# Kernel optimization log

Hardware: AMD Instinct MI355X
Metric: run time of the kernel (lower is better)

The kernel has to match this reference:

```python
import jax, jax.numpy as jnp
import numpy as np
import math

B, CH, BINS, W = 2, 8, 1024, 1024
FF = 2048
BANDS = 4
HD = BINS // BANDS
EPS = 1e-5


def _ln(x, g, b):
    m = jnp.mean(x, -1, keepdims=True)
    v = jnp.mean(jnp.square(x - m), -1, keepdims=True)
    return (x - m) * jax.lax.rsqrt(v + EPS) * g + b


def _conv1d(x, w, pad, groups=1):
    # x: [B, C, W], w: [O, I/groups, k]
    return jax.lax.conv_general_dilated(x, w, (1,), [(pad, pad)],
                                        dimension_numbers=('NCH', 'OIH', 'NCH'),
                                        feature_group_count=groups)


def _attn(h, mem, qw, qb, qcw, qcb, kw, kb, kcw, kcb, vw, vb, vcw, vcb, ow, ob, er):
    b, w, c = h.shape

    def proj(src, lw, lb, cw, cb):
        y = src @ lw.T + lb                                   # [b, w, c]
        y = _conv1d(y.transpose(0, 2, 1), cw, 1, groups=c) + cb[None, :, None]
        return y.transpose(0, 2, 1)                           # [b, w, c]

    q = proj(h, qw, qb, qcw, qcb).reshape(b, w, BANDS, HD).transpose(0, 2, 1, 3)   # [b, n, w, hd]
    k = proj(mem, kw, kb, kcw, kcb).reshape(b, w, BANDS, HD).transpose(0, 2, 1, 3)
    v = proj(mem, vw, vb, vcw, vcb).reshape(b, w, BANDS, HD).transpose(0, 2, 1, 3)
    # relative position bias via Music-Transformer pad/skew trick
    p = jnp.einsum('bnwh,hc->bnwc', q, er)                    # [b, n, w, W]
    p = jnp.pad(p, ((0, 0), (0, 0), (0, 0), (1, 0))).transpose(0, 1, 3, 2)[:, :, 1:, :]
    qk = (jnp.einsum('bnqh,bnkh->bnqk', q, k) + p) / math.sqrt(c)
    a = jax.nn.softmax(qk, axis=-1)
    o = jnp.einsum('bnqk,bnkh->bnqh', a, v).transpose(0, 2, 1, 3).reshape(b, w, c)
    return o @ ow.T + ob


def _forward(x, w_in, ln1_g, ln1_b, glu_w, ln2_g, ln2_b, c1L_w, c1R_w, ln3_g, ln3_b,
             c1M_dw, c1M_pw, ln4_g, ln4_b, qw, qb, qcw, qcb, kw, kb, kcw, kcb,
             vw, vb, vcw, vcb, ow, ob, er, ln5_g, ln5_b, c2_w, c3_w):
    # in_project: Linear(channels, 1, bias=False) on x.transpose(1,3), squeeze
    xf = jnp.einsum('bcfw,c->bwf', x, w_in)                   # [B, W, BINS]
    # GLU block
    h = _ln(xf, ln1_g, ln1_b)
    g = h @ glu_w.T
    ga, gb = jnp.split(g, 2, axis=-1)
    xf = xf + ga * jax.nn.sigmoid(gb)
    # conv feedforward block
    h = _ln(xf, ln2_g, ln2_b)
    hL = jax.nn.relu(h @ c1L_w.T)                             # [B, W, FF]
    hR = jax.nn.relu(_conv1d(h.transpose(0, 2, 1), c1R_w, 1)).transpose(0, 2, 1)  # [B, W, FF//4]
    hR = jnp.pad(hR, ((0, 0), (0, 0), (0, FF - FF // 4)))
    h = _ln(hL + hR, ln3_g, ln3_b)
    h = _conv1d(_conv1d(h.transpose(0, 2, 1), c1M_dw, 4, groups=FF), c1M_pw, 0).transpose(0, 2, 1)
    xf = xf + h
    # multiband attention
    h = _ln(xf, ln4_g, ln4_b)
    h = _attn(h, h, qw, qb, qcw, qcb, kw, kb, kcw, kcb, vw, vb, vcw, vcb, ow, ob, er)
    xf = xf + h
    # squared-relu FFN
    h = _ln(xf, ln5_g, ln5_b)
    h = jnp.square(jax.nn.relu(h @ c2_w.T)) @ c3_w.T
    xf = xf + h
    return xf.transpose(0, 2, 1)[:, None, :, :]               # [B, 1, BINS, W]


def setup_inputs() -> dict:
    key = jax.random.key(0)
    keys = iter(jax.random.split(key, 48))

    def n(shape, s=0.02):
        return jax.random.normal(next(keys), shape, dtype=jnp.float32) * s

    ones = lambda d: jnp.ones((d,), jnp.float32)
    zeros = lambda d: jnp.zeros((d,), jnp.float32)
    return {
        'x': jax.random.normal(next(keys), (B, CH, BINS, W), dtype=jnp.float32),
        'w_in': n((CH,)),
        'ln1_g': ones(BINS), 'ln1_b': zeros(BINS),
        'glu_w': n((2 * BINS, BINS)),
        'ln2_g': ones(BINS), 'ln2_b': zeros(BINS),
        'c1L_w': n((FF, BINS)),
        'c1R_w': n((FF // 4, BINS, 3)),
        'ln3_g': ones(FF), 'ln3_b': zeros(FF),
        'c1M_dw': n((FF, 1, 9)),
        'c1M_pw': n((BINS, FF, 1)),
        'ln4_g': ones(BINS), 'ln4_b': zeros(BINS),
        'qw': n((BINS, BINS)), 'qb': zeros(BINS), 'qcw': n((BINS, 1, 3)), 'qcb': zeros(BINS),
        'kw': n((BINS, BINS)), 'kb': zeros(BINS), 'kcw': n((BINS, 1, 3)), 'kcb': zeros(BINS),
        'vw': n((BINS, BINS)), 'vb': zeros(BINS), 'vcw': n((BINS, 1, 3)), 'vcb': zeros(BINS),
        'ow': n((BINS, BINS)), 'ob': zeros(BINS),
        'er': n((HD, W), s=1.0),
        'ln5_g': ones(BINS), 'ln5_b': zeros(BINS),
        'c2_w': n((FF, BINS)), 'c3_w': n((BINS, FF)),
    }


def reference(x, w_in, ln1_g, ln1_b, glu_w, ln2_g, ln2_b, c1L_w, c1R_w, ln3_g, ln3_b,
              c1M_dw, c1M_pw, ln4_g, ln4_b, qw, qb, qcw, qcb, kw, kb, kcw, kcb,
              vw, vb, vcw, vcb, ow, ob, er, ln5_g, ln5_b, c2_w, c3_w):
    return _forward(x, w_in, ln1_g, ln1_b, glu_w, ln2_g, ln2_b, c1L_w, c1R_w, ln3_g, ln3_b,
                    c1M_dw, c1M_pw, ln4_g, ln4_b, qw, qb, qcw, qcb, kw, kb, kcw, kcb,
                    vw, vb, vcw, vcb, ow, ob, er, ln5_g, ln5_b, c2_w, c3_w)
```

## Files before the change

### kernel.cpp

```cpp
#include <hip/hip_runtime.h>


typedef float f32x4 __attribute__((ext_vector_type(4)));
typedef short short8 __attribute__((ext_vector_type(8)));
typedef unsigned short u16;
typedef unsigned int u32;

__device__ __forceinline__ float bf2f(u16 u){
  u32 v = ((u32)u) << 16;
  return __builtin_bit_cast(float, v);
}
__device__ __forceinline__ u16 f2bf(float f){
  u32 u = __builtin_bit_cast(u32, f);
  u32 r = (u + 0x7fffu + ((u >> 16) & 1u)) >> 16;
  return (u16)r;
}
__device__ __forceinline__ u32 pack2(float a, float b){
  return (u32)f2bf(a) | ((u32)f2bf(b) << 16);
}
__device__ __forceinline__ void unpack8(uint4 u, float* f){
  f[0]=bf2f(u.x & 0xffffu); f[1]=bf2f(u.x >> 16);
  f[2]=bf2f(u.y & 0xffffu); f[3]=bf2f(u.y >> 16);
  f[4]=bf2f(u.z & 0xffffu); f[5]=bf2f(u.z >> 16);
  f[6]=bf2f(u.w & 0xffffu); f[7]=bf2f(u.w >> 16);
}

__device__ __forceinline__ void gload16(const u16* g, u16* l){
  __builtin_amdgcn_global_load_lds(
      (const __attribute__((address_space(1))) unsigned int*)g,
      (__attribute__((address_space(3))) unsigned int*)l, 16, 0, 0);
}
template<int N> __device__ __forceinline__ void waitvm(){
  asm volatile("s_waitcnt vmcnt(%0)" :: "n"(N) : "memory");
}
__device__ __forceinline__ void barrier(){ __builtin_amdgcn_s_barrier(); }

template<int ACT, int OB, int MR, int NR, int DUAL, int NBUF, int RB, int SC>
__device__ __forceinline__
void gemm_body(u16* ldsA, u16* ldsB,
               const u16* Az, const u16* Bz,
               const u16* A2, const u16* B2z,
               float* CfZ, u16* CbZ,
               const float* bias, const void* rz,
               int K, int K2, int lda, int ldb, int lda2, int ldb2, int ldc,
               int apad, int aoff, int m0, int n0)
{
  constexpr int BM = 32 * MR, BN = 32 * NR;
  constexpr int LPT = MR + NR;
  constexpr int PRE = NBUF - 1;
  const int tid = threadIdx.x;
  const int lane = tid & 63, wid = tid >> 6;
  const int wm = wid >> 1, wn = wid & 1;
  const int lr = lane & 15, lk = lane >> 4;
  const int kA = K >> 6;
  const int NT = kA + (DUAL ? (K2 >> 6) : 0);

  auto stage = [&](int buf, int s){
    #pragma unroll
    for (int i = 0; i < MR; i++){
      int ch = tid + i * 256;
      int r = ch >> 3, c = ch & 7;
      int csw = (c ^ (r & 7)) * 8;
      const u16* src;
      bool d2 = DUAL && (s >= kA);
      if (d2){
        src = A2 + (long)(m0 + r) * lda2 + (s - kA) * 64 + csw;
      } else {
        int gm = m0 + r;
        long ar = (long)gm + (long)(gm >> 10) * apad + aoff;
        src = Az + ar * lda + s * 64 + csw;
      }
      gload16(src, ldsA + buf * (BM * 64) + ch * 8);
    }
    #pragma unroll
    for (int i = 0; i < NR; i++){
      int ch = tid + i * 256;
      int r = ch >> 3, c = ch & 7;
      int csw = (c ^ (r & 7)) * 8;
      const u16* src;
      bool d2 = DUAL && (s >= kA);
      if (d2) src = B2z + (long)(n0 + r) * ldb2 + (s - kA) * 64 + csw;
      else    src = Bz  + (long)(n0 + r) * ldb  + s * 64 + csw;
      gload16(src, ldsB + buf * (BN * 64) + ch * 8);
    }
  };

  f32x4 acc[MR][NR];
  #pragma unroll
  for (int i = 0; i < MR; i++)
    #pragma unroll
    for (int j = 0; j < NR; j++) acc[i][j] = f32x4{0.f, 0.f, 0.f, 0.f};

  auto compute = [&](int cur){
    const u16* Ab = ldsA + cur * (BM * 64);
    const u16* Bb = ldsB + cur * (BN * 64);
    short8 av[2][MR], bv[2][NR];
    #pragma unroll
    for (int h = 0; h < 2; h++){
      int g = h * 4 + lk;
      #pragma unroll
      for (int i = 0; i < MR; i++){
        int row = wm * 16 * MR + i * 16 + lr;
        av[h][i] = *(const short8*)(Ab + row * 64 + ((g ^ (row & 7)) * 8));
      }
      #pragma unroll
      for (int j = 0; j < NR; j++){
        int row = wn * 16 * NR + j * 16 + lr;
        bv[h][j] = *(const short8*)(Bb + row * 64 + ((g ^ (row & 7)) * 8));
      }
    }
    #pragma unroll
    for (int h = 0; h < 2; h++)
      #pragma unroll
      for (int i = 0; i < MR; i++)
        #pragma unroll
        for (int j = 0; j < NR; j++)
          acc[i][j] = __builtin_amdgcn_mfma_f32_16x16x32_bf16(av[h][i], bv[h][j], acc[i][j], 0, 0, 0);
  };

  const int npre = NT < PRE ? NT : PRE;
  for (int p = 0; p < npre; p++) stage(p, p);
  int s = 0;
  for (; s < NT - PRE; s++){
    waitvm<(NBUF - 2) * LPT>();
    barrier();
    stage((s + PRE) % NBUF, s + PRE);
    compute(s % NBUF);
  }
  for (; s < NT; s++){
    waitvm<0>();
    barrier();
    compute(s % NBUF);
  }

  const float* rzf = (!RB) ? (const float*)rz : nullptr;
  const u16*  rzb = ( RB) ? (const u16*)rz  : nullptr;
  #pragma unroll
  for (int i = 0; i < MR; i++){
    int rowb = m0 + wm * 16 * MR + i * 16 + lk * 4;
    #pragma unroll
    for (int j = 0; j < NR; j++){
      int colg = n0 + wn * 16 * NR + j * 16 + lr;
      f32x4 v = acc[i][j];
      float bvl = bias ? bias[colg] : 0.f;
      #pragma unroll
      for (int r = 0; r < 4; r++){
        long idx = (long)(rowb + r) * ldc + colg;
        float xv = v[r] + bvl;
        if constexpr (ACT == 1){ xv = fmaxf(xv, 0.f); }
        if constexpr (ACT == 2){ xv = fmaxf(xv, 0.f); xv = xv * xv; }
        if constexpr (SC){ xv *= 0.03125f; }
        if constexpr (RB){ if (rzb) xv += bf2f(rzb[idx]); }
        else             { if (rzf) xv += rzf[idx]; }
        if constexpr (OB) CbZ[idx] = f2bf(xv); else CfZ[idx] = xv;
      }
    }
  }
}

template<int ACT, int OB, int MR, int NR, int DUAL, int NBUF, int RB, int SC>
__global__ __launch_bounds__(256)
void gemm_bt(const u16* __restrict__ A, const u16* __restrict__ Bw,
             const u16* __restrict__ A2, const u16* __restrict__ B2,
             float* __restrict__ Cf, u16* __restrict__ Cb,
             const float* __restrict__ bias, const void* __restrict__ resid,
             int M, int N, int K, int K2,
             int lda, int ldb, int lda2, int ldb2, int ldc,
             int apad, int aoff,
             long aZHi, long aZLo, long bZHi, long bZLo,
             long b2ZHi, long b2ZLo, long cZHi, long cZLo)
{
  constexpr int BM = 32 * MR, BN = 32 * NR;
  __shared__ __align__(16) u16 As[NBUF * BM * 64];
  __shared__ __align__(16) u16 Bs[NBUF * BN * 64];
  const int z = blockIdx.z, zh = z >> 2, zl = z & 3;
  const u16* Az = A + zh * aZHi + zl * aZLo;
  const u16* Bz = Bw + zh * bZHi + zl * bZLo;
  const u16* B2z = DUAL ? (B2 + zh * b2ZHi + zl * b2ZLo) : nullptr;
  const long coff = (long)zh * cZHi + (long)zl * cZLo;
  const int m0 = blockIdx.y * BM, n0 = blockIdx.x * BN;
  float* CfZ = Cf ? Cf + coff : nullptr;
  u16*  CbZ = Cb ? Cb + coff : nullptr;
  const void* rz = nullptr;
  if (resid) rz = RB ? (const void*)(((const u16*)resid) + coff)
                     : (const void*)(((const float*)resid) + coff);
  gemm_body<ACT,OB,MR,NR,DUAL,NBUF,RB,SC>(As, Bs, Az, Bz, A2, B2z, CfZ, CbZ,
      bias, rz, K, K2, lda, ldb, lda2, ldb2, ldc, apad, aoff, m0, n0);
}

__global__ __launch_bounds__(256)
void gemm_c1(const u16* __restrict__ HPAD, const u16* __restrict__ wbL,
             const u16* __restrict__ wbR, u16* __restrict__ HS, u16* __restrict__ HR)
{
  __shared__ __align__(16) u16 lds[24576];
  const int bid = blockIdx.x;
  if (bid < 512){
    const int n0 = (bid & 31) * 64, m0 = (bid >> 5) * 128;
    gemm_body<1,1,4,2,0,2,0,0>(lds, lds + 2 * 128 * 64,
        HPAD, wbL, nullptr, nullptr, nullptr, HS, nullptr, nullptr,
        1024, 0, 1024, 1024, 0, 0, 2048, 2, 1, m0, n0);
  } else {
    const int r = bid - 512;
    const int n0 = (r & 15) * 32, m0 = (r >> 4) * 64;
    gemm_body<1,1,2,1,0,4,0,0>(lds, lds + 4 * 64 * 64,
        HPAD, wbR, nullptr, nullptr, nullptr, HR, nullptr, nullptr,
        3072, 0, 1024, 3072, 0, 0, 512, 2, 0, m0, n0);
  }
}

template<int NBUF>
__global__ __launch_bounds__(256)
void gemm_glu(const u16* __restrict__ A, const u16* __restrict__ Bw,
              u16* __restrict__ XF)
{
  constexpr int LPT = 6;
  constexpr int PRE = NBUF - 1;
  constexpr int NT = 16;
  __shared__ __align__(16) u16 As[NBUF][64 * 64];
  __shared__ __align__(16) u16 Bs[NBUF][128 * 64];
  const int tid = threadIdx.x;
  const int m0 = blockIdx.y * 64, n0 = blockIdx.x * 64;
  const int lane = tid & 63, wid = tid >> 6;
  const int wm = wid >> 1, wn = wid & 1;
  const int lr = lane & 15, lk = lane >> 4;

  auto stage = [&](int buf, int s){
    #pragma unroll
    for (int i = 0; i < 2; i++){
      int ch = tid + i * 256;
      int r = ch >> 3, c = ch & 7;
      int csw = (c ^ (r & 7)) * 8;
      gload16(A + (long)(m0 + r) * 1024 + s * 64 + csw, &As[buf][ch * 8]);
    }
    #pragma unroll
    for (int i = 0; i < 4; i++){
      int ch = tid + i * 256;
      int r = ch >> 3, c = ch & 7;
      int csw = (c ^ (r & 7)) * 8;
      int grow = (r < 64) ? (n0 + r) : (1024 + n0 + r - 64);
      gload16(Bw + (long)grow * 1024 + s * 64 + csw, &Bs[buf][ch * 8]);
    }
  };

  f32x4 accv[2][2], accg[2][2];
  #pragma unroll
  for (int i = 0; i < 2; i++)
    #pragma unroll
    for (int j = 0; j < 2; j++){
      accv[i][j] = f32x4{0.f,0.f,0.f,0.f};
      accg[i][j] = f32x4{0.f,0.f,0.f,0.f};
    }

  auto compute = [&](int cur){
    const u16* Ab = &As[cur][0];
    const u16* Bb = &Bs[cur][0];
    short8 av[2][2], bvv[2][2], bvg[2][2];
    #pragma unroll
    for (int h = 0; h < 2; h++){
      int g = h * 4 + lk;
      #pragma unroll
      for (int i = 0; i < 2; i++){
        int row = wm * 32 + i * 16 + lr;
        av[h][i] = *(const short8*)(Ab + row * 64 + ((g ^ (row & 7)) * 8));
      }
      #pragma unroll
      for (int j = 0; j < 2; j++){
        int row = wn * 32 + j * 16 + lr;
        bvv[h][j] = *(const short8*)(Bb + row * 64 + ((g ^ (row & 7)) * 8));
        int rowg = 64 + row;
        bvg[h][j] = *(const short8*)(Bb + rowg * 64 + ((g ^ (rowg & 7)) * 8));
      }
    }
    #pragma unroll
    for (int h = 0; h < 2; h++)
      #pragma unroll
      for (int i = 0; i < 2; i++)
        #pragma unroll
        for (int j = 0; j < 2; j++){
          accv[i][j] = __builtin_amdgcn_mfma_f32_16x16x32_bf16(av[h][i], bvv[h][j], accv[i][j], 0, 0, 0);
          accg[i][j] = __builtin_amdgcn_mfma_f32_16x16x32_bf16(av[h][i], bvg[h][j], accg[i][j], 0, 0, 0);
        }
  };

  const int npre = NT < PRE ? NT : PRE;
  for (int p = 0; p < npre; p++) stage(p, p);
  int s = 0;
  for (; s < NT - PRE; s++){
    waitvm<(NBUF - 2) * LPT>();
    barrier();
    stage((s + PRE) % NBUF, s + PRE);
    compute(s % NBUF);
  }
  for (; s < NT; s++){
    waitvm<0>();
    barrier();
    compute(s % NBUF);
  }

  #pragma unroll
  for (int i = 0; i < 2; i++){
    int rowb = m0 + wm * 32 + i * 16 + lk * 4;
    #pragma unroll
    for (int j = 0; j < 2; j++){
      int colg = n0 + wn * 32 + j * 16 + lr;
      #pragma unroll
      for (int r = 0; r < 4; r++){
        long idx = (long)(rowb + r) * 1024 + colg;
        float g = accg[i][j][r];
        float nv = bf2f(XF[idx]) + accv[i][j][r] / (1.f + __expf(-g));
        XF[idx] = f2bf(nv);
      }
    }
  }
}

template<int NC, int INBF, int ADDHR>
__global__ __launch_bounds__(256)
void ln_kernel(const void* __restrict__ in, u16* __restrict__ out,
               const float* __restrict__ gg, const float* __restrict__ bb,
               int rowpad, int rowadd, const u16* __restrict__ addp)
{
  constexpr int PER = NC / 256;
  const int row = blockIdx.x;
  const int tid = threadIdx.x;
  float v[PER];
  if constexpr (INBF){
    const u16* x = ((const u16*)in) + (long)row * NC + tid * PER;
    if constexpr (PER == 4){
      uint2 u = *(const uint2*)x;
      v[0]=bf2f(u.x & 0xffffu); v[1]=bf2f(u.x >> 16);
      v[2]=bf2f(u.y & 0xffffu); v[3]=bf2f(u.y >> 16);
    } else {
      #pragma unroll
      for (int i = 0; i < PER; i += 8){
        uint4 u = *(const uint4*)(x + i);
        unpack8(u, &v[i]);
      }
    }
  } else {
    const float* x = ((const float*)in) + (long)row * NC + tid * PER;
    #pragma unroll
    for (int i = 0; i < PER; i += 4){
      f32x4 t = *(const f32x4*)(x + i);
      v[i] = t.x; v[i+1] = t.y; v[i+2] = t.z; v[i+3] = t.w;
    }
  }
  if constexpr (ADDHR){
    const int c0i = tid * PER;
    if (c0i < 512){
      uint4 u = *(const uint4*)(addp + (long)row * 512 + c0i);
      float a8[8]; unpack8(u, a8);
      #pragma unroll
      for (int i = 0; i < 8; i++) v[i] += a8[i];
    }
  }
  float s = 0.f, sq = 0.f;
  #pragma unroll
  for (int i = 0; i < PER; i++){ s += v[i]; sq += v[i] * v[i]; }
  #pragma unroll
  for (int o = 32; o; o >>= 1){ s += __shfl_xor(s, o); sq += __shfl_xor(sq, o); }
  __shared__ float as_[4], aq_[4];
  const int wv = tid >> 6;
  if ((tid & 63) == 0){ as_[wv] = s; aq_[wv] = sq; }
  __syncthreads();
  s  = as_[0] + as_[1] + as_[2] + as_[3];
  sq = aq_[0] + aq_[1] + aq_[2] + aq_[3];
  const float mean = s * (1.f / NC);
  const float var  = sq * (1.f / NC) - mean * mean;
  const float rs = rsqrtf(var + 1e-5f);
  const long orow = (long)row + (long)(row >> 10) * rowpad + rowadd;
  u16* op = out + orow * NC + tid * PER;
  u32 word[PER / 2];
  #pragma unroll
  for (int i = 0; i < PER; i += 2){
    int c = tid * PER + i;
    float y0 = (v[i]   - mean) * rs * gg[c]   + bb[c];
    float y1 = (v[i+1] - mean) * rs * gg[c+1] + bb[c+1];
    word[i / 2] = pack2(y0, y1);
  }
  if constexpr (PER == 4) *(uint2*)op = *(uint2*)word;
  else                    *(uint4*)op = *(uint4*)word;
}

__global__ __launch_bounds__(256)
void tr_out_kernel(const u16* __restrict__ xf, float* __restrict__ out)
{
  __shared__ float tile[32][33];
  const int b = blockIdx.z, f0 = blockIdx.x * 32, w0 = blockIdx.y * 32;
  const int tx = threadIdx.x, ty = threadIdx.y;
  #pragma unroll
  for (int i = 0; i < 4; i++)
    tile[ty + i * 8][tx] = bf2f(xf[((long)(b * 1024 + w0 + ty + i * 8)) * 1024 + f0 + tx]);
  __syncthreads();
  #pragma unroll
  for (int i = 0; i < 4; i++)
    out[((long)(b * 1024 + f0 + ty + i * 8)) * 1024 + w0 + tx] = tile[tx][ty + i * 8];
}

__global__ __launch_bounds__(256)
void dwconv9_kernel(const u16* __restrict__ in, u16* __restrict__ out,
                    const float* __restrict__ dwT)
{
  const int id = blockIdx.x * 256 + threadIdx.x;
  const int cg = id & 255;
  const int tg = id >> 8;
  const int c0 = cg * 8;
  const int t0 = tg * 4;
  const int b = t0 >> 10;
  const int w0 = t0 & 1023;
  const u16* bin = in + ((long)b << 10) * 2048 + c0;
  float wt[9][8];
  #pragma unroll
  for (int j = 0; j < 9; j++){
    f32x4 lo = *(const f32x4*)(dwT + j * 2048 + c0);
    f32x4 hi = *(const f32x4*)(dwT + j * 2048 + c0 + 4);
    wt[j][0]=lo.x; wt[j][1]=lo.y; wt[j][2]=lo.z; wt[j][3]=lo.w;
    wt[j][4]=hi.x; wt[j][5]=hi.y; wt[j][6]=hi.z; wt[j][7]=hi.w;
  }
  float win[9][8];
  #pragma unroll
  for (int r = 0; r < 9; r++){
    int wr = w0 - 4 + r;
    if (wr >= 0 && wr < 1024){
      uint4 u = *(const uint4*)(bin + (long)wr * 2048);
      unpack8(u, win[r]);
    } else {
      #pragma unroll
      for (int i = 0; i < 8; i++) win[r][i] = 0.f;
    }
  }
  #pragma unroll
  for (int s = 0; s < 4; s++){
    float acc[8] = {0,0,0,0,0,0,0,0};
    #pragma unroll
    for (int j = 0; j < 9; j++)
      #pragma unroll
      for (int i = 0; i < 8; i++)
        acc[i] += win[(s + j) % 9][i] * wt[j][i];
    uint4 o;
    o.x = pack2(acc[0], acc[1]); o.y = pack2(acc[2], acc[3]);
    o.z = pack2(acc[4], acc[5]); o.w = pack2(acc[6], acc[7]);
    *(uint4*)(out + (long)(t0 + s) * 2048 + c0) = o;
    if (s < 3){
      int wr = w0 + s + 5;
      if (wr < 1024){
        uint4 u = *(const uint4*)(bin + (long)wr * 2048);
        unpack8(u, win[s % 9]);
      } else {
        #pragma unroll
        for (int i = 0; i < 8; i++) win[s % 9][i] = 0.f;
      }
    }
  }
}

__global__ __launch_bounds__(256)
void qkvconv_kernel(const u16* __restrict__ qkv,
                    u16* __restrict__ q2b, const float* __restrict__ qwT, const float* __restrict__ qbb,
                    u16* __restrict__ k2b, const float* __restrict__ kwT, const float* __restrict__ kbb,
                    u16* __restrict__ v2T, const float* __restrict__ vcw, const float* __restrict__ vcb)
{
  __shared__ float ins[34][33];
  __shared__ float outs[32][33];
  const int bid = blockIdx.x;
  const int tid = threadIdx.x;
  if (bid < 512){
    const int sel = bid >> 8;
    const u16* in  = qkv + sel * 1024;
    u16* out       = sel ? k2b : q2b;
    const float* wT = sel ? kwT : qwT;
    const float* bp = sel ? kbb : qbb;
    const int id = (bid & 255) * 256 + tid;
    const int cg = id & 127;
    const int tg = id >> 7;
    const int c0 = cg * 8;
    const int t0 = tg * 4;
    const int b = t0 >> 10;
    const int w0 = t0 & 1023;
    const u16* bin = in + ((long)b << 10) * 3072 + c0;
    float wt[3][8], bias[8];
    #pragma unroll
    for (int j = 0; j < 3; j++){
      f32x4 lo = *(const f32x4*)(wT + j * 1024 + c0);
      f32x4 hi = *(const f32x4*)(wT + j * 1024 + c0 + 4);
      wt[j][0]=lo.x; wt[j][1]=lo.y; wt[j][2]=lo.z; wt[j][3]=lo.w;
      wt[j][4]=hi.x; wt[j][5]=hi.y; wt[j][6]=hi.z; wt[j][7]=hi.w;
    }
    {
      f32x4 lo = *(const f32x4*)(bp + c0);
      f32x4 hi = *(const f32x4*)(bp + c0 + 4);
      bias[0]=lo.x; bias[1]=lo.y; bias[2]=lo.z; bias[3]=lo.w;
      bias[4]=hi.x; bias[5]=hi.y; bias[6]=hi.z; bias[7]=hi.w;
    }
    float win[3][8];
    #pragma unroll
    for (int r = 0; r < 3; r++){
      int wr = w0 - 1 + r;
      if (wr >= 0 && wr < 1024){
        uint4 u = *(const uint4*)(bin + (long)wr * 3072);
        unpack8(u, win[r]);
      } else {
        #pragma unroll
        for (int i = 0; i < 8; i++) win[r][i] = 0.f;
      }
    }
    #pragma unroll
    for (int s = 0; s < 4; s++){
      float acc[8];
      #pragma unroll
      for (int i = 0; i < 8; i++) acc[i] = bias[i];
      #pragma unroll
      for (int j = 0; j < 3; j++)
        #pragma unroll
        for (int i = 0; i < 8; i++)
          acc[i] += win[(s + j) % 3][i] * wt[j][i];
      uint4 o;
      o.x = pack2(acc[0], acc[1]); o.y = pack2(acc[2], acc[3]);
      o.z = pack2(acc[4], acc[5]); o.w = pack2(acc[6], acc[7]);
      *(uint4*)(out + (long)(t0 + s) * 1024 + c0) = o;
      if (s < 3){
        int wr = w0 + s + 2;
        if (wr < 1024){
          uint4 u = *(const uint4*)(bin + (long)wr * 3072);
          unpack8(u, win[s % 3]);
        } else {
          #pragma unroll
          for (int i = 0; i < 8; i++) win[s % 3][i] = 0.f;
        }
      }
    }
  } else {
    const int vb = bid - 512;
    const int b = vb >> 10;
    const int rem = vb & 1023;
    const int w0 = (rem & 31) * 32, c0 = (rem >> 5) * 32;
    const int tx = tid & 31, ty = tid >> 5;
    const u16* in = qkv + 2048;
    for (int r = ty; r < 34; r += 8){
      int w = w0 - 1 + r;
      ins[r][tx] = (w >= 0 && w < 1024) ? bf2f(in[((long)(b * 1024 + w)) * 3072 + c0 + tx]) : 0.f;
    }
    __syncthreads();
    const float wt0 = vcw[(c0 + tx) * 3 + 0], wt1 = vcw[(c0 + tx) * 3 + 1], wt2 = vcw[(c0 + tx) * 3 + 2];
    const float bb = vcb[c0 + tx];
    #pragma unroll
    for (int i = 0; i < 4; i++){
      int wl = ty + i * 8;
      outs[wl][tx] = ins[wl][tx] * wt0 + ins[wl + 1][tx] * wt1 + ins[wl + 2][tx] * wt2 + bb;
    }
    __syncthreads();
    #pragma unroll
    for (int i = 0; i < 4; i++){
      int cl = ty + i * 8;
      int c = c0 + cl; int n = c >> 8; int h = c & 255;
      v2T[((long)((b * 4 + n) * 256 + h)) * 1024 + w0 + tx] = f2bf(outs[tx][cl]);
    }
  }
}

__global__ __launch_bounds__(256)
void softmax_kernel(u16* __restrict__ buf)
{
  const long row = (long)blockIdx.x * 4 + (threadIdx.x >> 6);
  const int lane = threadIdx.x & 63;
  u16* p = buf + row * 1024 + lane * 16;
  uint4 a = *(const uint4*)p;
  uint4 b = *(const uint4*)(p + 8);
  float v[16];
  unpack8(a, v); unpack8(b, v + 8);
  float m = v[0];
  #pragma unroll
  for (int i = 1; i < 16; i++) m = fmaxf(m, v[i]);
  #pragma unroll
  for (int o = 32; o; o >>= 1) m = fmaxf(m, __shfl_xor(m, o));
  float e[16];
  float s = 0.f;
  #pragma unroll
  for (int i = 0; i < 16; i++){ e[i] = __expf(v[i] - m); s += e[i]; }
  #pragma unroll
  for (int o = 32; o; o >>= 1) s += __shfl_xor(s, o);
  const float inv = 1.f / s;
  u32 w[8];
  #pragma unroll
  for (int i = 0; i < 16; i += 2) w[i / 2] = pack2(e[i] * inv, e[i + 1] * inv);
  *(uint4*)p = *(uint4*)&w[0];
  *(uint4*)(p + 8) = *(uint4*)&w[4];
}

struct Ptrs9 { const float* s[9]; u16* d[9]; };

__global__ __launch_bounds__(256)
void prep_all_kernel(Ptrs9 p,
                     const float* __restrict__ c1R_w, u16* __restrict__ wb_c1R,
                     const float* __restrict__ er, u16* __restrict__ wb_erT,
                     const float* __restrict__ c1M_dw, float* __restrict__ dwT,
                     const float* __restrict__ qcw, float* __restrict__ qcwT,
                     const float* __restrict__ kcw, float* __restrict__ kcwT,
                     const float* __restrict__ qb, const float* __restrict__ kb,
                     const float* __restrict__ vb, float* __restrict__ bqkv,
                     u16* __restrict__ hpad,
                     const float* __restrict__ x, const float* __restrict__ w_in,
                     u16* __restrict__ XF)
{
  __shared__ float tile[32][33];
  const int tid = threadIdx.x;
  const int bid = blockIdx.x;
  if (bid < 7168){
    int job, base;
    if      (bid < 1024){ job = 0; base = 0; }
    else if (bid < 2048){ job = 1; base = 1024; }
    else if (bid < 3072){ job = 2; base = 2048; }
    else if (bid < 3584){ job = 3; base = 3072; }
    else if (bid < 4096){ job = 4; base = 3584; }
    else if (bid < 4608){ job = 5; base = 4096; }
    else if (bid < 5120){ job = 6; base = 4608; }
    else if (bid < 6144){ job = 7; base = 5120; }
    else                { job = 8; base = 6144; }
    long off = ((long)(bid - base) * 256 + tid) * 8;
    const float* src = p.s[job] + off;
    f32x4 va = *(const f32x4*)src;
    f32x4 vb4 = *(const f32x4*)(src + 4);
    uint4 o;
    o.x = pack2(va.x, va.y); o.y = pack2(va.z, va.w);
    o.z = pack2(vb4.x, vb4.y); o.w = pack2(vb4.z, vb4.w);
    *(uint4*)(p.d[job] + off) = o;
    return;
  }
  const int b2 = bid - 7168;
  if (b2 < 2048){
    int t = b2 * 256 + tid;
    int oc = t >> 10, ic = t & 1023;
    const float* src = c1R_w + (long)oc * 3072 + ic * 3;
    float r0 = src[0], r1 = src[1], r2 = src[2];
    u16* dst = wb_c1R + (long)oc * 3072 + ic;
    dst[0]    = f2bf(r0);
    dst[1024] = f2bf(r1);
    dst[2048] = f2bf(r2);
  } else if (b2 < 2304){
    int r = b2 - 2048;
    int h0 = (r & 7) * 32, q0 = (r >> 3) * 32;
    int tx = tid & 31, ty = tid >> 5;
    #pragma unroll
    for (int i = 0; i < 4; i++)
      tile[ty + i * 8][tx] = er[(long)(h0 + ty + i * 8) * 1024 + q0 + tx];
    __syncthreads();
    #pragma unroll
    for (int i = 0; i < 4; i++)
      wb_erT[(long)(q0 + ty + i * 8) * 256 + h0 + tx] = f2bf(tile[tx][ty + i * 8]);
  } else if (b2 < 2312){
    int c = (b2 - 2304) * 256 + tid;
    const float* src = c1M_dw + (long)c * 9;
    #pragma unroll
    for (int j = 0; j < 9; j++) dwT[j * 2048 + c] = src[j];
  } else if (b2 < 2316){
    int c = (b2 - 2312) * 256 + tid;
    const float* src = qcw + (long)c * 3;
    #pragma unroll
    for (int j = 0; j < 3; j++) qcwT[j * 1024 + c] = src[j];
  } else if (b2 < 2320){
    int c = (b2 - 2316) * 256 + tid;
    const float* src = kcw + (long)c * 3;
    #pragma unroll
    for (int j = 0; j < 3; j++) kcwT[j * 1024 + c] = src[j];
  } else if (b2 < 2332){
    int id = (b2 - 2320) * 256 + tid;
    bqkv[id] = (id < 1024) ? qb[id] : (id < 2048) ? kb[id - 1024] : vb[id - 2048];
  } else if (b2 < 2348){
    int id = (b2 - 2332) * 256 + tid;
    int r = id >> 10; int c = id & 1023;
    int b = r >> 1; int edge = r & 1;
    long row = (long)b * 1026 + (edge ? 1025 : 0);
    hpad[row * 1024 + c] = 0;
  } else {
    const int vb4 = b2 - 2348;
    const int b = vb4 >> 10;
    const int rem = vb4 & 1023;
    const int f0 = (rem & 31) * 32, w0 = (rem >> 5) * 32;
    const int tx = tid & 7, ty = tid >> 3;
    float wr[8];
    #pragma unroll
    for (int c = 0; c < 8; c++) wr[c] = w_in[c];
    f32x4 acc = f32x4{0.f, 0.f, 0.f, 0.f};
    #pragma unroll
    for (int c = 0; c < 8; c++){
      f32x4 xv = *(const f32x4*)(x + (((long)(b * 8 + c)) * 1024 + f0 + ty) * 1024 + w0 + tx * 4);
      acc += wr[c] * xv;
    }
    tile[ty][tx * 4 + 0] = acc.x;
    tile[ty][tx * 4 + 1] = acc.y;
    tile[ty][tx * 4 + 2] = acc.z;
    tile[ty][tx * 4 + 3] = acc.w;
    __syncthreads();
    const int wl = tid >> 3, fseg = (tid & 7) * 4;
    uint2 o;
    o.x = pack2(tile[fseg + 0][wl], tile[fseg + 1][wl]);
    o.y = pack2(tile[fseg + 2][wl], tile[fseg + 3][wl]);
    *(uint2*)(XF + ((long)(b * 1024 + w0 + wl)) * 1024 + f0 + fseg) = o;
  }
}

extern "C" void kernel_launch(void* const* d_in, const int* in_sizes, int n_in,
                              void* d_out, int out_size, void* d_ws, size_t ws_size,
                              hipStream_t stream)
{
  (void)in_sizes; (void)n_in; (void)out_size; (void)ws_size;
  const float* x     = (const float*)d_in[0];
  const float* w_in  = (const float*)d_in[1];
  const float* ln1_g = (const float*)d_in[2];
  const float* ln1_b = (const float*)d_in[3];
  const float* glu_w = (const float*)d_in[4];
  const float* ln2_g = (const float*)d_in[5];
  const float* ln2_b = (const float*)d_in[6];
  const float* c1L_w = (const float*)d_in[7];
  const float* c1R_w = (const float*)d_in[8];
  const float* ln3_g = (const float*)d_in[9];
  const float* ln3_b = (const float*)d_in[10];
  const float* c1M_dw= (const float*)d_in[11];
  const float* c1M_pw= (const float*)d_in[12];
  const float* ln4_g = (const float*)d_in[13];
  const float* ln4_b = (const float*)d_in[14];
  const float* qw  = (const float*)d_in[15];
  const float* qb  = (const float*)d_in[16];
  const float* qcw = (const float*)d_in[17];
  const float* qcb = (const float*)d_in[18];
  const float* kw  = (const float*)d_in[19];
  const float* kb  = (const float*)d_in[20];
  const float* kcw = (const float*)d_in[21];
  const float* kcb = (const float*)d_in[22];
  const float* vw  = (const float*)d_in[23];
  const float* vb  = (const float*)d_in[24];
  const float* vcw = (const float*)d_in[25];
  const float* vcb = (const float*)d_in[26];
  const float* ow  = (const float*)d_in[27];
  const float* ob  = (const float*)d_in[28];
  const float* er  = (const float*)d_in[29];
  const float* ln5_g = (const float*)d_in[30];
  const float* ln5_b = (const float*)d_in[31];
  const float* c2_w  = (const float*)d_in[32];
  const float* c3_w  = (const float*)d_in[33];
  float* out = (float*)d_out;

  const long TT = 2048;
  char* wsb = (char*)d_ws;
  size_t off = 0;
  auto alloc = [&](size_t bytes) -> char* {
    char* p = wsb + off;
    off = (off + bytes + 255) & ~(size_t)255;
    return p;
  };
  u16* XF     = (u16*)alloc(TT * 1024 * 2);
  u16* wb_glu = (u16*)alloc(2048L * 1024 * 2);
  u16* wb_c1L = (u16*)alloc(2048L * 1024 * 2);
  u16* wb_c1R = (u16*)alloc(512L * 3072 * 2);
  u16* wb_pw  = (u16*)alloc(1024L * 2048 * 2);
  u16* wb_q   = (u16*)alloc(1024L * 1024 * 2);
  u16* wb_k   = (u16*)alloc(1024L * 1024 * 2);
  u16* wb_v   = (u16*)alloc(1024L * 1024 * 2);
  u16* wb_ow  = (u16*)alloc(1024L * 1024 * 2);
  u16* wb_c2  = (u16*)alloc(2048L * 1024 * 2);
  u16* wb_c3  = (u16*)alloc(1024L * 2048 * 2);
  u16* wb_erT = (u16*)alloc(1024L * 256 * 2);
  float* dwT  = (float*)alloc(9L * 2048 * 4);
  float* qcwT = (float*)alloc(3L * 1024 * 4);
  float* kcwT = (float*)alloc(3L * 1024 * 4);
  float* bqkv = (float*)alloc(3072L * 4);
  u16* HPAD   = (u16*)alloc(2L * 1026 * 1024 * 2);
  u16* LNA    = (u16*)alloc(TT * 1024 * 2);
  u16* HS     = (u16*)alloc(TT * 2048 * 2);
  u16* HR     = (u16*)alloc(TT * 512 * 2);
  u16* LN3O   = (u16*)alloc(TT * 2048 * 2);
  u16* DW9O   = (u16*)alloc(TT * 2048 * 2);
  u16* SBF    = (u16*)alloc(8L * 1024 * 1024 * 2);
  u16* qkvbuf = (u16*)alloc(TT * 3072 * 2);
  u16* q2b  = (u16*)alloc(TT * 1024 * 2);
  u16* k2b  = (u16*)alloc(TT * 1024 * 2);
  u16* v2T  = (u16*)alloc(8L * 256 * 1024 * 2);
  u16* obuf = qkvbuf;
  u16* C2O  = LN3O;

  Ptrs9 pj;
  pj.s[0]=glu_w; pj.d[0]=wb_glu;
  pj.s[1]=c1L_w; pj.d[1]=wb_c1L;
  pj.s[2]=c1M_pw; pj.d[2]=wb_pw;
  pj.s[3]=qw; pj.d[3]=wb_q;
  pj.s[4]=kw; pj.d[4]=wb_k;
  pj.s[5]=vw; pj.d[5]=wb_v;
  pj.s[6]=ow; pj.d[6]=wb_ow;
  pj.s[7]=c2_w; pj.d[7]=wb_c2;
  pj.s[8]=c3_w; pj.d[8]=wb_c3;
  prep_all_kernel<<<11564, 256, 0, stream>>>(pj, c1R_w, wb_c1R, er, wb_erT, c1M_dw, dwT,
                                             qcw, qcwT, kcw, kcwT, qb, kb, vb, bqkv, HPAD,
                                             x, w_in, XF);

  ln_kernel<1024,1,0><<<2048, 256, 0, stream>>>(XF, LNA, ln1_g, ln1_b, 0, 0, nullptr);
  gemm_glu<2><<<dim3(16,32,1), 256, 0, stream>>>(LNA, wb_glu, XF);

  ln_kernel<1024,1,0><<<2048, 256, 0, stream>>>(XF, HPAD, ln2_g, ln2_b, 2, 1, nullptr);
  gemm_c1<<<1024, 256, 0, stream>>>(HPAD, wb_c1L, wb_c1R, HS, HR);
  ln_kernel<2048,1,1><<<2048, 256, 0, stream>>>(HS, LN3O, ln3_g, ln3_b, 0, 0, HR);
  dwconv9_kernel<<<512, 256, 0, stream>>>(LN3O, DW9O, dwT);
  gemm_bt<0,1,2,2,0,3,1,0><<<dim3(16,32,1), 256, 0, stream>>>(DW9O, wb_pw, nullptr, nullptr,
      nullptr, XF, nullptr, XF,
      2048, 1024, 2048, 0, 2048, 2048, 0, 0, 1024, 0, 0, 0,0,0,0,0,0,0,0);

  ln_kernel<1024,1,0><<<2048, 256, 0, stream>>>(XF, LNA, ln4_g, ln4_b, 0, 0, nullptr);
  gemm_bt<0,1,4,2,0,2,0,0><<<dim3(48,16,1), 256, 0, stream>>>(LNA, wb_q, nullptr, nullptr,
      nullptr, qkvbuf, bqkv, nullptr,
      2048, 3072, 1024, 0, 1024, 1024, 0, 0, 3072, 0, 0, 0,0,0,0,0,0,0,0);
  qkvconv_kernel<<<2560, 256, 0, stream>>>(qkvbuf, q2b, qcwT, qcb, k2b, kcwT, kcb,
                                           v2T, vcw, vcb);
  gemm_bt<0,1,2,2,1,3,0,1><<<dim3(16,16,8), 256, 0, stream>>>(q2b, k2b, wb_erT, q2b,
      nullptr, SBF, nullptr, nullptr,
      1024, 1024, 256, 256, 1024, 1024, 256, 1024, 1024, 0, 0,
      1048576, 256, 1048576, 256, 1048576, 256, 4194304, 1048576);
  softmax_kernel<<<2048, 256, 0, stream>>>(SBF);
  gemm_bt<0,1,1,2,0,4,0,0><<<dim3(4,32,8), 256, 0, stream>>>(SBF, v2T, nullptr, nullptr,
      nullptr, obuf, nullptr, nullptr,
      1024, 256, 1024, 0, 1024, 1024, 0, 0, 1024, 0, 0,
      4194304, 1048576, 1048576, 262144, 0, 0, 1048576, 256);
  gemm_bt<0,1,2,2,0,3,1,0><<<dim3(16,32,1), 256, 0, stream>>>(obuf, wb_ow, nullptr, nullptr,
      nullptr, XF, ob, XF,
      2048, 1024, 1024, 0, 1024, 1024, 0, 0, 1024, 0, 0, 0,0,0,0,0,0,0,0);

  ln_kernel<1024,1,0><<<2048, 256, 0, stream>>>(XF, LNA, ln5_g, ln5_b, 0, 0, nullptr);
  gemm_bt<2,1,4,2,0,2,0,0><<<dim3(32,16,1), 256, 0, stream>>>(LNA, wb_c2, nullptr, nullptr,
      nullptr, C2O, nullptr, nullptr,
      2048, 2048, 1024, 0, 1024, 1024, 0, 0, 2048, 0, 0, 0,0,0,0,0,0,0,0);
  gemm_bt<0,1,2,2,0,3,1,0><<<dim3(16,32,1), 256, 0, stream>>>(C2O, wb_c3, nullptr, nullptr,
      nullptr, XF, nullptr, XF,
      2048, 1024, 2048, 0, 2048, 2048, 0, 0, 1024, 0, 0, 0,0,0,0,0,0,0,0);

  tr_out_kernel<<<dim3(32, 32, 2), dim3(32, 8), 0, stream>>>(XF, out);
}
```

Before: 281.0 us.

## Fuse row softmax into attention-times-V GEMM kernel

Replaces the separate in-place softmax pass over the score matrix and the following generic GEMM with a single kernel. Each block loads 32 full score rows into LDS, normalizes them there into a swizzled layout, then runs MFMA against double-buffered V tiles. This removes one full read and write of the bf16 score tensor. The cost is that each of the 4 column blocks per row group recomputes the softmax, and the 64KB+ of LDS per block limits occupancy.

```diff
diff --git a/kernel.cpp b/kernel.cpp
--- a/kernel.cpp
+++ b/kernel.cpp
@@ -311,6 +311,102 @@
         XF[idx] = f2bf(nv);
       }
     }
+  }
+}
+
+__global__ __launch_bounds__(256)
+void fused_av(const u16* __restrict__ S, const u16* __restrict__ V,
+              u16* __restrict__ O)
+{
+  __shared__ __align__(16) u16 P[32 * 1024];
+  __shared__ __align__(16) u16 Bs[2][64 * 64];
+  const int z = blockIdx.z;
+  const int m0 = blockIdx.y * 32;
+  const int n0 = blockIdx.x * 64;
+  const int tid = threadIdx.x;
+  const int lane = tid & 63, wid = tid >> 6;
+  const int wm = wid >> 1, wn = wid & 1;
+  const int lr = lane & 15, lk = lane >> 4;
+  const u16* Sz = S + (long)z * 1048576 + (long)m0 * 1024;
+  const u16* Vz = V + (long)z * 262144;
+
+  auto stageB = [&](int buf, int s){
+    #pragma unroll
+    for (int i = 0; i < 2; i++){
+      int ch = tid + i * 256;
+      int r = ch >> 3, c = ch & 7;
+      int csw = (c ^ (r & 7)) * 8;
+      gload16(Vz + (long)(n0 + r) * 1024 + s * 64 + csw, &Bs[buf][ch * 8]);
+    }
+  };
+
+  #pragma unroll
+  for (int i = 0; i < 16; i++){
+    int ch = tid + i * 256;
+    gload16(Sz + ch * 8, &P[ch * 8]);
+  }
+  stageB(0, 0);
+  waitvm<2>();
+  barrier();
+
+  #pragma unroll
+  for (int i = 0; i < 8; i++){
+    int row = wid * 8 + i;
+    const u16* pr = &P[row * 1024 + lane * 16];
+    uint4 a = *(const uint4*)pr;
+    uint4 b = *(const uint4*)(pr + 8);
+    float v[16];
+    unpack8(a, v); unpack8(b, v + 8);
+    float m = v[0];
+    #pragma unroll
+    for (int j = 1; j < 16; j++) m = fmaxf(m, v[j]);
+    #pragma unroll
+    for (int o = 32; o; o >>= 1) m = fmaxf(m, __shfl_xor(m, o));
+    float sm = 0.f;
+    #pragma unroll
+    for (int j = 0; j < 16; j++){ v[j] = __expf(v[j] - m); sm += v[j]; }
+    #pragma unroll
+    for (int o = 32; o; o >>= 1) sm += __shfl_xor(sm, o);
+    const float inv = 1.f / sm;
+    u32 w[8];
+    #pragma unroll
+    for (int j = 0; j < 16; j += 2) w[j / 2] = pack2(v[j] * inv, v[j + 1] * inv);
+    const int x = row & 7;
+    const int cc = lane * 2;
+    *(uint4*)&P[row * 1024 + ((cc       ^ x)) * 8] = *(uint4*)&w[0];
+    *(uint4*)&P[row * 1024 + (((cc + 1) ^ x)) * 8] = *(uint4*)&w[4];
+  }
+  barrier();
+
+  f32x4 acc[2];
+  acc[0] = f32x4{0.f,0.f,0.f,0.f};
+  acc[1] = f32x4{0.f,0.f,0.f,0.f};
+  for (int s = 0; s < 16; s++){
+    waitvm<0>();
+    barrier();
+    if (s + 1 < 16) stageB((s + 1) & 1, s + 1);
+    const u16* Bb = &Bs[s & 1][0];
+    const int arow = wm * 16 + lr;
+    #pragma unroll
+    for (int h = 0; h < 2; h++){
+      int g = h * 4 + lk;
+      short8 av = *(const short8*)&P[arow * 1024 + s * 64 + ((g ^ (arow & 7)) * 8)];
+      #pragma unroll
+      for (int j = 0; j < 2; j++){
+        int brow = wn * 32 + j * 16 + lr;
+        short8 bv = *(const short8*)(Bb + brow * 64 + ((g ^ (brow & 7)) * 8));
+        acc[j] = __builtin_amdgcn_mfma_f32_16x16x32_bf16(av, bv, acc[j], 0, 0, 0);
+      }
+    }
+  }
+
+  const int rowb = (z >> 2) * 1024 + m0 + wm * 16 + lk * 4;
+  #pragma unroll
+  for (int j = 0; j < 2; j++){
+    int colg = (z & 3) * 256 + n0 + wn * 32 + j * 16 + lr;
+    #pragma unroll
+    for (int r = 0; r < 4; r++)
+      O[(long)(rowb + r) * 1024 + colg] = f2bf(acc[j][r]);
   }
 }
 
@@ -556,35 +652,6 @@
       v2T[((long)((b * 4 + n) * 256 + h)) * 1024 + w0 + tx] = f2bf(outs[tx][cl]);
     }
   }
-}
-
-__global__ __launch_bounds__(256)
-void softmax_kernel(u16* __restrict__ buf)
-{
-  const long row = (long)blockIdx.x * 4 + (threadIdx.x >> 6);
-  const int lane = threadIdx.x & 63;
-  u16* p = buf + row * 1024 + lane * 16;
-  uint4 a = *(const uint4*)p;
-  uint4 b = *(const uint4*)(p + 8);
-  float v[16];
-  unpack8(a, v); unpack8(b, v + 8);
-  float m = v[0];
-  #pragma unroll
-  for (int i = 1; i < 16; i++) m = fmaxf(m, v[i]);
-  #pragma unroll
-  for (int o = 32; o; o >>= 1) m = fmaxf(m, __shfl_xor(m, o));
-  float e[16];
-  float s = 0.f;
-  #pragma unroll
-  for (int i = 0; i < 16; i++){ e[i] = __expf(v[i] - m); s += e[i]; }
-  #pragma unroll
-  for (int o = 32; o; o >>= 1) s += __shfl_xor(s, o);
-  const float inv = 1.f / s;
-  u32 w[8];
-  #pragma unroll
-  for (int i = 0; i < 16; i += 2) w[i / 2] = pack2(e[i] * inv, e[i + 1] * inv);
-  *(uint4*)p = *(uint4*)&w[0];
-  *(uint4*)(p + 8) = *(uint4*)&w[4];
 }
 
 struct Ptrs9 { const float* s[9]; u16* d[9]; };
@@ -813,11 +880,7 @@
       nullptr, SBF, nullptr, nullptr,
       1024, 1024, 256, 256, 1024, 1024, 256, 1024, 1024, 0, 0,
       1048576, 256, 1048576, 256, 1048576, 256, 4194304, 1048576);
-  softmax_kernel<<<2048, 256, 0, stream>>>(SBF);
-  gemm_bt<0,1,1,2,0,4,0,0><<<dim3(4,32,8), 256, 0, stream>>>(SBF, v2T, nullptr, nullptr,
-      nullptr, obuf, nullptr, nullptr,
-      1024, 256, 1024, 0, 1024, 1024, 0, 0, 1024, 0, 0,
-      4194304, 1048576, 1048576, 262144, 0, 0, 1048576, 256);
+  fused_av<<<dim3(4,32,8), 256, 0, stream>>>(SBF, v2T, obuf);
   gemm_bt<0,1,2,2,0,3,1,0><<<dim3(16,32,1), 256, 0, stream>>>(obuf, wb_ow, nullptr, nullptr,
       nullptr, XF, ob, XF,
       2048, 1024, 1024, 0, 1024, 1024, 0, 0, 1024, 0, 0, 0,0,0,0,0,0,0,0);
```

Result: slower. 291.8 us (+3.8%).
